# Optimization experiments

Measured on AMD Instinct MI355X. Metric: run time of the kernel, lower is better.

The kernel has to match this reference:

```python
import jax, jax.numpy as jnp
import numpy as np
from jax import lax

BATCH = 256
N_LAGS = 512
RD = 256          # reservoir_dim
NOISE_DIM = 32    # input_dim == noise_input_dim
HID = 32          # hidden_dim
INIT_NOISE = 30   # initial_noise_dim
N_PAST = 128      # length of conditioning past path


def setup_inputs() -> dict:
    key = jax.random.key(0)
    ks = jax.random.split(key, 32)
    n = lambda i, shape, scale=1.0: jax.random.normal(ks[i], shape, dtype=jnp.float32) * scale
    s = 1.0 / np.sqrt(RD).astype(np.float32)
    return {
        "batch_size": BATCH,
        "n_lags": N_LAGS,
        "x_past": n(0, (N_PAST, 1)),
        "V_noise": n(1, (BATCH, NOISE_DIM)),
        "increments": n(2, (BATCH, N_LAGS, 1)),
        # initial-condition network 1 (noise -> initial_noise_dim)
        "W1h": n(3, (HID, NOISE_DIM), 1.0 / np.sqrt(NOISE_DIM)),
        "b1h": n(4, (HID,), 0.1),
        "W1o": n(5, (INIT_NOISE, HID), 1.0 / np.sqrt(HID)),
        "b1o": n(6, (INIT_NOISE,), 0.1),
        # initial-condition network 2 (rsig -> rd - initial_noise_dim)
        "W2h": n(7, (HID, RD), 1.0 / np.sqrt(RD)),
        "b2h": n(8, (HID,), 0.1),
        "W2o": n(9, (RD - INIT_NOISE, HID), 1.0 / np.sqrt(HID)),
        "b2o": n(10, (RD - INIT_NOISE,), 0.1),
        # SDE reservoir parameters
        "rho1": n(11, ()),
        "rho2": n(12, ()),
        "rho3": n(13, ()),
        "rho4": n(14, ()),
        "B1": n(15, (RD, RD), s),
        "B2": n(16, (RD, RD), s),
        "lam1": n(17, (RD,)),
        "lam2": n(18, (RD,)),
        # conditioning (randomized-signature) reservoir parameters
        "A1": n(19, (RD, RD), s),
        "A2": n(20, (RD, RD), s),
        "xi1": n(21, (RD,)),
        "xi2": n(22, (RD,)),
        # readout
        "Wr": n(23, (1, RD), 1.0 / np.sqrt(RD)),
        "br": n(24, (1,), 0.1),
    }


def reference(batch_size, n_lags, x_past, V_noise, increments,
              W1h, b1h, W1o, b1o, W2h, b2h, W2o, b2o,
              rho1, rho2, rho3, rho4, B1, B2, lam1, lam2,
              A1, A2, xi1, xi2, Wr, br):
    act = jnp.tanh
    rd = B1.shape[0]

    # ---- initial condition V from noise ----
    V = act(V_noise @ W1h.T + b1h) @ W1o.T + b1o            # (B, INIT_NOISE)

    # ---- randomized signature of the past path (compute_rsig) ----
    dx = x_past[1:, 0] - x_past[:-1, 0]                      # (N_PAST-1,)

    def rsig_step(Z, dxt):
        Zn = Z + act(A1 @ Z + xi1) + act(A2 @ Z + xi2) * dxt
        return Zn, None

    Z, _ = lax.scan(rsig_step, jnp.zeros((rd,), jnp.float32), dx)
    rsig = act(Z @ W2h.T + b2h) @ W2o.T + b2o                # (rd - INIT_NOISE,)
    rsig_b = jnp.broadcast_to(rsig[None, :], (batch_size, rsig.shape[0]))

    # ---- initial reservoir state R_0 = [rsig_cond; V] ----
    R0 = jnp.concatenate([rsig_b, V], axis=1)                # (B, rd)

    # ---- Brownian path: cumsum with W[:,0]=0, then increments ----
    Wp = jnp.cumsum(increments, axis=1)
    Wp = Wp.at[:, 0, :].set(0.0)
    dW = Wp[:, 1:, 0] - Wp[:, :-1, 0]                        # (B, n_lags-1)

    # ---- sequential SDE reservoir recurrence ----
    def sde_step(R, dWt):  # R: (B, rd), dWt: (B,)
        drift = act(rho1 * (R @ B1.T) + rho2 * lam1)
        diffu = act(rho3 * (R @ B2.T) + rho4 * lam2)
        Rn = R + drift + diffu * dWt[:, None]
        return Rn, Rn

    _, Rs = lax.scan(sde_step, R0, dW.T)                     # (n_lags-1, B, rd)
    Rall = jnp.concatenate([R0[None], Rs], axis=0)           # (n_lags, B, rd)

    # ---- linear readout at every lag ----
    x = jnp.einsum('tbr,or->tbo', Rall, Wr) + br             # (n_lags, B, 1)
    x = jnp.transpose(x, (1, 0, 2))                          # (B, n_lags, 1)
    return x
```

## Files before the change

### kernel.cpp

```cpp
#include <hip/hip_runtime.h>

typedef __attribute__((ext_vector_type(4))) float f32x4;
typedef __attribute__((ext_vector_type(2))) float f32x2;

#define RD 256
#define NLAGS 512
#define NPAST 128

__device__ __forceinline__ float ftanh(float x) {
    float ax = __builtin_fabsf(x);
    float e = __builtin_amdgcn_exp2f(ax * 2.8853900817779268f);
    float r = 1.0f - 2.0f * __builtin_amdgcn_rcpf(e + 1.0f);
    return __builtin_copysignf(r, x);
}

__device__ __forceinline__ unsigned pkh(_Float16 lo, _Float16 hi) {
    unsigned a = (unsigned)__builtin_bit_cast(unsigned short, lo);
    unsigned b = (unsigned)__builtin_bit_cast(unsigned short, hi);
    return a | (b << 16);
}

#define DPPADD(v, ctrl) { int _t = __builtin_amdgcn_update_dpp(0, __float_as_int(v), ctrl, 0xf, 0xf, true); \
                          (v) += __int_as_float(_t); }
#define QUADSUM(v) DPPADD(v, 0xB1) DPPADD(v, 0x4E)

#define RPT16(M) M(0) M(1) M(2) M(3) M(4) M(5) M(6) M(7) M(8) M(9) M(10) M(11) M(12) M(13) M(14) M(15)
#define RPTP(M) M(0,0,1) M(1,2,3) M(2,4,5) M(3,6,7) M(4,8,9) M(5,10,11) M(6,12,13) M(7,14,15)

#define DECL_W(c) \
    f32x2 w##c##_01, w##c##_23, w##c##_45, w##c##_67; \
    unsigned hA_##c, hB_##c, hC_##c, hD_##c; \
    unsigned lwA_##c, lwB_##c;

#define STG(c) { \
    int off = (((c) << 4) + q64) & 0xF0; \
    f32x4 a0 = *(const f32x4*)(pB1 + off); \
    f32x4 a1 = *(const f32x4*)(pB1 + 1024 + off); \
    w##c##_01 = f32x2{a0[0]*sc1, a0[1]*sc1}; \
    w##c##_23 = f32x2{a0[2]*sc1, a0[3]*sc1}; \
    w##c##_45 = f32x2{a1[0]*sc1, a1[1]*sc1}; \
    w##c##_67 = f32x2{a1[2]*sc1, a1[3]*sc1}; \
    f32x4 e0 = *(const f32x4*)(pB2 + off) * sc2; \
    f32x4 e1 = *(const f32x4*)(pB2 + 1024 + off) * sc2; \
    _Float16 h0=(_Float16)e0[0], h1=(_Float16)e0[1], h2=(_Float16)e0[2], h3=(_Float16)e0[3]; \
    _Float16 h4=(_Float16)e1[0], h5=(_Float16)e1[1], h6=(_Float16)e1[2], h7=(_Float16)e1[3]; \
    hA_##c = pkh(h0,h1); hB_##c = pkh(h2,h3); hC_##c = pkh(h4,h5); hD_##c = pkh(h6,h7); \
    float l0=(e0[0]-(float)h0)*4096.f, l1=(e0[1]-(float)h1)*4096.f; \
    float l2=(e0[2]-(float)h2)*4096.f, l3=(e0[3]-(float)h3)*4096.f; \
    float m0=(e1[0]-(float)h4)*4096.f, m1=(e1[1]-(float)h5)*4096.f; \
    float m2=(e1[2]-(float)h6)*4096.f, m3=(e1[3]-(float)h7)*4096.f; \
    unsigned uA = (unsigned)__builtin_amdgcn_cvt_pk_fp8_f32(l0, l1, 0, false); \
    uA = (unsigned)__builtin_amdgcn_cvt_pk_fp8_f32(l2, l3, (int)uA, true); \
    unsigned uB = (unsigned)__builtin_amdgcn_cvt_pk_fp8_f32(m0, m1, 0, false); \
    uB = (unsigned)__builtin_amdgcn_cvt_pk_fp8_f32(m2, m3, (int)uB, true); \
    lwA_##c = uA; lwB_##c = uB; }

#define KEEPW(c) asm volatile("" : \
    "+v"(w##c##_01), "+v"(w##c##_23), "+v"(w##c##_45), "+v"(w##c##_67), \
    "+v"(hA_##c), "+v"(hB_##c), "+v"(hC_##c), "+v"(hD_##c));

#define STO(p, c0, c1) lo_lds[((p) << 9) + tid] = make_uint4(lwA_##c0, lwB_##c0, lwA_##c1, lwB_##c1);

#define PKFMA(acc, w, r) asm("v_pk_fma_f32 %0, %1, %2, %0" : "+v"(acc) : "v"(w), "v"(r));
#define MIXLO(acc, u, r) asm("v_fma_mix_f32 %0, %1, %2, %0 op_sel_hi:[1,0,0]" : "+v"(acc) : "v"(u), "v"(r));
#define MIXHI(acc, u, r) asm("v_fma_mix_f32 %0, %1, %2, %0 op_sel:[1,0,0] op_sel_hi:[1,0,0]" : "+v"(acc) : "v"(u), "v"(r));

#define F4L(accv, w, rv01, rv23) { \
    f32x2 pA_ = __builtin_amdgcn_cvt_pk_f32_fp8((int)(w), false); \
    f32x2 pB_ = __builtin_amdgcn_cvt_pk_f32_fp8((int)(w), true); \
    PKFMA(accv, pA_, rv01) \
    PKFMA(accv, pB_, rv23) }

#define DOT1(c, wA, wB) { \
    f32x4 rv = *(const f32x4*)(RqR + ((((c) << 4) + q64) & 0xF0)); \
    f32x2 rv01 = f32x2{rv[0], rv[1]}; \
    f32x2 rv23 = f32x2{rv[2], rv[3]}; \
    PKFMA(acc1_0v, w##c##_01, rv01) PKFMA(acc1_0v, w##c##_23, rv23) \
    PKFMA(acc1_1v, w##c##_45, rv01) PKFMA(acc1_1v, w##c##_67, rv23) \
    MIXLO(acc2_0, hA_##c, rv[0]) MIXHI(acc2_0, hA_##c, rv[1]) \
    MIXLO(acc2_0, hB_##c, rv[2]) MIXHI(acc2_0, hB_##c, rv[3]) \
    MIXLO(acc2_1, hC_##c, rv[0]) MIXHI(acc2_1, hC_##c, rv[1]) \
    MIXLO(acc2_1, hD_##c, rv[2]) MIXHI(acc2_1, hD_##c, rv[3]) \
    F4L(accl_0v, wA, rv01, rv23) F4L(accl_1v, wB, rv01, rv23) }

#define DOTP(p, c0, c1) { \
    uint4 Lq = lo_lds[((p) << 9) + tid]; \
    const unsigned* Lw = (const unsigned*)&Lq; \
    DOT1(c0, Lw[0], Lw[1]) \
    DOT1(c1, Lw[2], Lw[3]) }

#define SCLF (1.0f / 4096.0f)

__global__ __attribute__((amdgpu_num_vgpr(256), amdgpu_waves_per_eu(2, 2)))
void __launch_bounds__(512) sde_main_kernel(
    const float* __restrict__ inc, const float* __restrict__ Vn,
    const float* __restrict__ W1h, const float* __restrict__ b1h,
    const float* __restrict__ W1o, const float* __restrict__ b1o,
    const float* __restrict__ rho1p, const float* __restrict__ rho2p,
    const float* __restrict__ rho3p, const float* __restrict__ rho4p,
    const float* __restrict__ B1, const float* __restrict__ B2,
    const float* __restrict__ lam1, const float* __restrict__ lam2,
    const float* __restrict__ Wr, const float* __restrict__ brp,
    const float* __restrict__ rsig, float* __restrict__ out)
{
    const int tid  = threadIdx.x;
    const int b    = blockIdx.x;
    const int q    = tid & 3;
    const int g    = tid >> 2;
    const int lane = tid & 63;
    const int wvi  = tid >> 6;
    const int q64  = q << 6;
    const int myrow = 2 * g + (q & 1);

    __shared__ __align__(16) uint4 lo_lds[8 * 512];
    __shared__ __align__(16) float Rs[2][RD];
    __shared__ __align__(16) float inc_lds[NLAGS];
    __shared__ float red[2][8];
    __shared__ float hv[32];

    const float rho1 = *rho1p, rho2 = *rho2p, rho3 = *rho3p, rho4 = *rho4p;

    RPT16(DECL_W)
    {
        const float sc1 = rho1, sc2 = rho3;
        const char* pB1 = (const char*)(B1 + (2 * g) * RD) + (q << 8);
        const char* pB2 = (const char*)(B2 + (2 * g) * RD) + (q << 8);
        RPT16(STG)
        RPTP(STO)
    }
    RPT16(KEEPW)

    const float c1m  = rho2 * lam1[myrow];
    const float c2m  = rho4 * lam2[myrow];
    const float wrim = Wr[myrow];
    const float brv  = *brp;

    inc_lds[tid] = inc[b * NLAGS + tid];
    if (tid < 32) {
        float a = b1h[tid];
        const float* wrow = W1h + tid * 32;
        const float* vn = Vn + b * 32;
        for (int k = 0; k < 32; ++k) a = __builtin_fmaf(wrow[k], vn[k], a);
        hv[tid] = ftanh(a);
    }
    if (tid < RD - 30) ((float*)Rs)[tid] = rsig[tid];
    __syncthreads();
    if (tid == 0) inc_lds[1] = inc_lds[0] + inc_lds[1];
    if (tid < 30) {
        float a = b1o[tid];
        const float* wrow = W1o + tid * 32;
        for (int k = 0; k < 32; ++k) a = __builtin_fmaf(wrow[k], hv[k], a);
        ((float*)Rs)[(RD - 30) + tid] = a;
    }
    __syncthreads();

    float rmine = ((const float*)Rs)[myrow];

    {
        float p = (q < 2) ? rmine * wrim : 0.0f;
        QUADSUM(p)
        p += __shfl_xor(p, 4, 64);
        p += __shfl_xor(p, 8, 64);
        p += __shfl_xor(p, 16, 64);
        p += __shfl_xor(p, 32, 64);
        if (lane == 0) red[0][wvi] = p;
    }
    __syncthreads();
    if (wvi == 0) {
        float s = (lane < 8) ? red[0][lane] : 0.0f;
        s += __shfl_xor(s, 1, 64);
        s += __shfl_xor(s, 2, 64);
        s += __shfl_xor(s, 4, 64);
        if (lane == 0) out[(size_t)b * NLAGS] = s + brv;
    }

    char* RsB = (char*)Rs;
    int rbase = 0;
    float* outp = out + (size_t)b * NLAGS;

#pragma unroll 1
    for (int t = 0; t < NLAGS - 1; ++t) {
        const float dwt = inc_lds[t + 1];
        const char* RqR = RsB + rbase + (q << 8);
        f32x2 acc1_0v = f32x2{0.f, 0.f}, acc1_1v = f32x2{0.f, 0.f};
        f32x2 accl_0v = f32x2{0.f, 0.f}, accl_1v = f32x2{0.f, 0.f};
        float acc2_0 = 0.f, acc2_1 = 0.f;
        RPTP(DOTP)
        float a1_0 = acc1_0v[0] + acc1_0v[1];
        float a1_1 = acc1_1v[0] + acc1_1v[1];
        float a2_0 = __builtin_fmaf(accl_0v[0] + accl_0v[1], SCLF, acc2_0);
        float a2_1 = __builtin_fmaf(accl_1v[0] + accl_1v[1], SCLF, acc2_1);
        QUADSUM(a1_0) QUADSUM(a1_1) QUADSUM(a2_0) QUADSUM(a2_1)
        float s1 = (q & 1) ? a1_1 : a1_0;
        float s2 = (q & 1) ? a2_1 : a2_0;
        float rn = rmine + ftanh(s1 + c1m) + ftanh(s2 + c2m) * dwt;
        rmine = rn;
        if (q < 2) *(float*)(RsB + (rbase ^ 1024) + myrow * 4) = rn;
        float p = (q < 2) ? rn * wrim : 0.0f;
        QUADSUM(p)
        p += __shfl_xor(p, 4, 64);
        p += __shfl_xor(p, 8, 64);
        p += __shfl_xor(p, 16, 64);
        p += __shfl_xor(p, 32, 64);
        const int slot = (t + 1) & 1;
        if (lane == 0) red[slot][wvi] = p;
        __syncthreads();
        if (wvi == 0) {
            float s = (lane < 8) ? red[slot][lane] : 0.0f;
            s += __shfl_xor(s, 1, 64);
            s += __shfl_xor(s, 2, 64);
            s += __shfl_xor(s, 4, 64);
            if (lane == 0) outp[t + 1] = s + brv;
        }
        rbase ^= 1024;
    }
}

__global__ __attribute__((amdgpu_num_vgpr(256), amdgpu_waves_per_eu(2, 2)))
void __launch_bounds__(512) rsig_kernel(
    const float* __restrict__ xp,
    const float* __restrict__ A1, const float* __restrict__ A2,
    const float* __restrict__ xi1, const float* __restrict__ xi2,
    const float* __restrict__ W2h, const float* __restrict__ b2h,
    const float* __restrict__ W2o, const float* __restrict__ b2o,
    float* __restrict__ rsig_out)
{
    const int tid = threadIdx.x;
    const int q   = tid & 3;
    const int g   = tid >> 2;
    const int q64 = q << 6;
    const int myrow = 2 * g + (q & 1);

    __shared__ __align__(16) uint4 lo_lds[8 * 512];
    __shared__ __align__(16) float Rs[2][RD];
    __shared__ float dx_lds[NPAST];
    __shared__ float Zlin[RD];
    __shared__ float hh[32];

    RPT16(DECL_W)
    {
        const float sc1 = 1.0f, sc2 = 1.0f;
        const char* pB1 = (const char*)(A1 + (2 * g) * RD) + (q << 8);
        const char* pB2 = (const char*)(A2 + (2 * g) * RD) + (q << 8);
        RPT16(STG)
        RPTP(STO)
    }
    RPT16(KEEPW)

    const float x1m = xi1[myrow];
    const float x2m = xi2[myrow];

    if (tid < NPAST - 1) dx_lds[tid] = xp[tid + 1] - xp[tid];
    ((float*)Rs)[tid] = 0.0f;
    __syncthreads();

    float zmine = 0.0f;
    char* RsB = (char*)Rs;
    int rbase = 0;

#pragma unroll 1
    for (int t = 0; t < NPAST - 1; ++t) {
        const float dxt = dx_lds[t];
        const char* RqR = RsB + rbase + (q << 8);
        f32x2 acc1_0v = f32x2{0.f, 0.f}, acc1_1v = f32x2{0.f, 0.f};
        f32x2 accl_0v = f32x2{0.f, 0.f}, accl_1v = f32x2{0.f, 0.f};
        float acc2_0 = 0.f, acc2_1 = 0.f;
        RPTP(DOTP)
        float a1_0 = acc1_0v[0] + acc1_0v[1];
        float a1_1 = acc1_1v[0] + acc1_1v[1];
        float a2_0 = __builtin_fmaf(accl_0v[0] + accl_0v[1], SCLF, acc2_0);
        float a2_1 = __builtin_fmaf(accl_1v[0] + accl_1v[1], SCLF, acc2_1);
        QUADSUM(a1_0) QUADSUM(a1_1) QUADSUM(a2_0) QUADSUM(a2_1)
        float s1 = (q & 1) ? a1_1 : a1_0;
        float s2 = (q & 1) ? a2_1 : a2_0;
        zmine = zmine + ftanh(s1 + x1m) + ftanh(s2 + x2m) * dxt;
        if (q < 2) *(float*)(RsB + (rbase ^ 1024) + myrow * 4) = zmine;
        __syncthreads();
        rbase ^= 1024;
    }

    if (q < 2) Zlin[myrow] = zmine;
    __syncthreads();

    if (tid < 32) {
        float a = b2h[tid];
        const float* wrow = W2h + tid * RD;
        for (int k = 0; k < RD; ++k) a = __builtin_fmaf(wrow[k], Zlin[k], a);
        hh[tid] = ftanh(a);
    }
    __syncthreads();
    if (tid < RD - 30) {
        float a = b2o[tid];
        const float* wrow = W2o + tid * 32;
        for (int k = 0; k < 32; ++k) a = __builtin_fmaf(wrow[k], hh[k], a);
        rsig_out[tid] = a;
    }
}

extern "C" void kernel_launch(void* const* d_in, const int* in_sizes, int n_in,
                              void* d_out, int out_size, void* d_ws, size_t ws_size,
                              hipStream_t stream) {
    const float* x_past  = (const float*)d_in[2];
    const float* V_noise = (const float*)d_in[3];
    const float* inc     = (const float*)d_in[4];
    const float* W1h     = (const float*)d_in[5];
    const float* b1h     = (const float*)d_in[6];
    const float* W1o     = (const float*)d_in[7];
    const float* b1o     = (const float*)d_in[8];
    const float* W2h     = (const float*)d_in[9];
    const float* b2h     = (const float*)d_in[10];
    const float* W2o     = (const float*)d_in[11];
    const float* b2o     = (const float*)d_in[12];
    const float* rho1    = (const float*)d_in[13];
    const float* rho2    = (const float*)d_in[14];
    const float* rho3    = (const float*)d_in[15];
    const float* rho4    = (const float*)d_in[16];
    const float* B1      = (const float*)d_in[17];
    const float* B2      = (const float*)d_in[18];
    const float* lam1    = (const float*)d_in[19];
    const float* lam2    = (const float*)d_in[20];
    const float* A1      = (const float*)d_in[21];
    const float* A2      = (const float*)d_in[22];
    const float* xi1     = (const float*)d_in[23];
    const float* xi2     = (const float*)d_in[24];
    const float* Wr      = (const float*)d_in[25];
    const float* br      = (const float*)d_in[26];

    float* rsig_ws = (float*)d_ws;

    rsig_kernel<<<1, 512, 0, stream>>>(x_past, A1, A2, xi1, xi2,
                                       W2h, b2h, W2o, b2o, rsig_ws);

    sde_main_kernel<<<256, 512, 0, stream>>>(inc, V_noise, W1h, b1h, W1o, b1o,
                                             rho1, rho2, rho3, rho4,
                                             B1, B2, lam1, lam2, Wr, br,
                                             rsig_ws, (float*)d_out);
}
```

Baseline: 1.193 ms.

## Defer readout reduction to kernel end and move barrier off the critical path

The per-step readout reduction no longer needs a second cross-wave combine inside the recurrence loop. Each wave now reduces its partial with a DPP row-broadcast chain, and its result is stored into a per-timestep LDS array of 512x8 entries. All 512 outputs are then summed in parallel once the loop ends. The barrier moves to just after the state write, so the readout reduction overlaps with the next step's dot products rather than sitting in front of the barrier. This costs 16KB of extra LDS, and it relies on the DPP row_bcast semantics leaving the full sum in lane 63.

Result: faster. 1.153 ms (-3.4%).

```diff
diff --git a/kernel.cpp b/kernel.cpp
--- a/kernel.cpp
+++ b/kernel.cpp
@@ -23,6 +23,8 @@
 #define DPPADD(v, ctrl) { int _t = __builtin_amdgcn_update_dpp(0, __float_as_int(v), ctrl, 0xf, 0xf, true); \
                           (v) += __int_as_float(_t); }
 #define QUADSUM(v) DPPADD(v, 0xB1) DPPADD(v, 0x4E)
+#define WSUM(v) DPPADD(v, 0x111) DPPADD(v, 0x112) DPPADD(v, 0x114) DPPADD(v, 0x118) \
+                DPPADD(v, 0x142) DPPADD(v, 0x143)
 
 #define RPT16(M) M(0) M(1) M(2) M(3) M(4) M(5) M(6) M(7) M(8) M(9) M(10) M(11) M(12) M(13) M(14) M(15)
 #define RPTP(M) M(0,0,1) M(1,2,3) M(2,4,5) M(3,6,7) M(4,8,9) M(5,10,11) M(6,12,13) M(7,14,15)
@@ -115,7 +117,7 @@
     __shared__ __align__(16) uint4 lo_lds[8 * 512];
     __shared__ __align__(16) float Rs[2][RD];
     __shared__ __align__(16) float inc_lds[NLAGS];
-    __shared__ float red[2][8];
+    __shared__ __align__(16) float red[NLAGS][8];
     __shared__ float hv[32];
 
     const float rho1 = *rho1p, rho2 = *rho2p, rho3 = *rho3p, rho4 = *rho4p;
@@ -158,20 +160,8 @@
 
     {
         float p = (q < 2) ? rmine * wrim : 0.0f;
-        QUADSUM(p)
-        p += __shfl_xor(p, 4, 64);
-        p += __shfl_xor(p, 8, 64);
-        p += __shfl_xor(p, 16, 64);
-        p += __shfl_xor(p, 32, 64);
-        if (lane == 0) red[0][wvi] = p;
-    }
-    __syncthreads();
-    if (wvi == 0) {
-        float s = (lane < 8) ? red[0][lane] : 0.0f;
-        s += __shfl_xor(s, 1, 64);
-        s += __shfl_xor(s, 2, 64);
-        s += __shfl_xor(s, 4, 64);
-        if (lane == 0) out[(size_t)b * NLAGS] = s + brv;
+        WSUM(p)
+        if (lane == 63) red[0][wvi] = p;
     }
 
     char* RsB = (char*)Rs;
@@ -196,23 +186,20 @@
         float rn = rmine + ftanh(s1 + c1m) + ftanh(s2 + c2m) * dwt;
         rmine = rn;
         if (q < 2) *(float*)(RsB + (rbase ^ 1024) + myrow * 4) = rn;
+        __syncthreads();
         float p = (q < 2) ? rn * wrim : 0.0f;
-        QUADSUM(p)
-        p += __shfl_xor(p, 4, 64);
-        p += __shfl_xor(p, 8, 64);
-        p += __shfl_xor(p, 16, 64);
-        p += __shfl_xor(p, 32, 64);
-        const int slot = (t + 1) & 1;
-        if (lane == 0) red[slot][wvi] = p;
-        __syncthreads();
-        if (wvi == 0) {
-            float s = (lane < 8) ? red[slot][lane] : 0.0f;
-            s += __shfl_xor(s, 1, 64);
-            s += __shfl_xor(s, 2, 64);
-            s += __shfl_xor(s, 4, 64);
-            if (lane == 0) outp[t + 1] = s + brv;
-        }
+        WSUM(p)
+        if (lane == 63) red[t + 1][wvi] = p;
         rbase ^= 1024;
+    }
+    __syncthreads();
+
+    {
+        float s = brv;
+        const float* rr = red[tid];
+#pragma unroll
+        for (int k = 0; k < 8; ++k) s += rr[k];
+        outp[tid] = s;
     }
 }
 
```
